# Kernel tuning notes

Measured on AMD Instinct MI355X. Metric: run time of the kernel, lower is better.

The kernel has to match this reference:

```python
import jax, jax.numpy as jnp
import numpy as np

NUM_NODES = 15000


def _gcn_conv(x, W, b, src, dst, norm, num_nodes):
    # PyG GCNConv: x' = D^-1/2 (A + I) D^-1/2 (x W) + b
    h = x @ W                                   # [N, out]
    msg = h[src] * norm[:, None]                # gather + scale per edge
    out = jax.ops.segment_sum(msg, dst, num_segments=num_nodes)
    return out + b


def setup_inputs() -> dict:
    key = jax.random.key(0)
    ks = jax.random.split(key, 12)
    T = 100000
    E = 200000
    inp = {
        "x": jax.random.normal(ks[0], (NUM_NODES, 768), jnp.float32),
        "r_emb": jax.random.normal(ks[1], (T, 768), jnp.float32),
        "W1": jax.random.normal(ks[2], (768, 10), jnp.float32) * 0.05,
        "b1": jax.random.normal(ks[3], (10,), jnp.float32) * 0.05,
        "W2": jax.random.normal(ks[4], (10, 128), jnp.float32) * 0.05,
        "b2": jax.random.normal(ks[5], (128,), jnp.float32) * 0.05,
        "W_ih": jax.random.normal(ks[6], (512, 1024), jnp.float32) * 0.03,
        "W_hh": jax.random.normal(ks[7], (512, 128), jnp.float32) * 0.03,
        "b_ih": jax.random.normal(ks[8], (512,), jnp.float32) * 0.03,
        "b_hh": jax.random.normal(ks[9], (512,), jnp.float32) * 0.03,
        "edge_index": jax.random.randint(ks[10], (2, E), 0, NUM_NODES).astype(jnp.int64),
        "triples": jax.random.randint(ks[11], (T, 3), 0, NUM_NODES).astype(jnp.int64),
    }
    return inp


def reference(x, r_emb, W1, b1, W2, b2, W_ih, W_hh, b_ih, b_hh, edge_index, triples):
    N = x.shape[0]
    H = 128  # lstm hidden size
    # --- add self loops, symmetric GCN normalization ---
    loop = jnp.arange(N, dtype=edge_index.dtype)
    src = jnp.concatenate([edge_index[0], loop])
    dst = jnp.concatenate([edge_index[1], loop])
    deg = jax.ops.segment_sum(jnp.ones_like(dst, jnp.float32), dst, num_segments=N)
    dinv = jnp.where(deg > 0, jax.lax.rsqrt(deg), 0.0)
    norm = dinv[src] * dinv[dst]                      # [E+N]
    # --- 2-layer GCN ---
    h = jax.nn.relu(_gcn_conv(x, W1, b1, src, dst, norm, N))   # [N, 10]
    z = _gcn_conv(h, W2, b2, src, dst, norm, N)                # [N, 128]
    # --- per-triple LSTM scoring, batched (seq_len=1, zero init state) ---
    hvec = z[triples[:, 0]]                           # [T, 128]
    tvec = z[triples[:, 2]]                           # [T, 128]
    feat = jnp.concatenate([hvec, r_emb, tvec], axis=-1)       # [T, 1024]
    gates = feat @ W_ih.T + (b_ih + b_hh)             # [T, 512]; h0=0 so W_hh term vanishes
    i_g, f_g, g_g, o_g = jnp.split(gates, 4, axis=-1)  # torch gate order i,f,g,o
    c = jax.nn.sigmoid(i_g) * jnp.tanh(g_g)           # c0 = 0 -> forget term drops
    out = jax.nn.sigmoid(o_g) * jnp.tanh(c)           # [T, 128]
    score = jax.nn.sigmoid(jnp.sum(out, axis=-1))     # [T]
    return score
```

## Files before the change

### kernel.cpp

```cpp
#include <hip/hip_runtime.h>

#define NF 768
#define D1 10
#define D2 128
#define BM 64

typedef __attribute__((ext_vector_type(8))) short bf16x8;
typedef __attribute__((ext_vector_type(16))) float f32x16;

static __device__ __forceinline__ float sigf(float v){ return 1.0f/(1.0f+__expf(-v)); }
static __device__ __forceinline__ float tanhfast(float v){ return 2.0f/(1.0f+__expf(-2.0f*v)) - 1.0f; }
static __device__ __forceinline__ short f2bf(float f){
    unsigned u = __float_as_uint(f);
    u += 0x7fffu + ((u>>16)&1u);
    return (short)(u>>16);
}

static __device__ __forceinline__ void gload16(const void* g, void* l){
    __builtin_amdgcn_global_load_lds(
        (const __attribute__((address_space(1))) unsigned int*)(unsigned long long)g,
        (__attribute__((address_space(3))) unsigned int*)(unsigned long long)l,
        16, 0, 0);
}

static __device__ __forceinline__ bf16x8 cvt8(float4 a, float4 b){
    unsigned u0,u1,u2,u3;
    asm("v_cvt_pk_bf16_f32 %0, %1, %2" : "=v"(u0) : "v"(a.x), "v"(a.y));
    asm("v_cvt_pk_bf16_f32 %0, %1, %2" : "=v"(u1) : "v"(a.z), "v"(a.w));
    asm("v_cvt_pk_bf16_f32 %0, %1, %2" : "=v"(u2) : "v"(b.x), "v"(b.y));
    asm("v_cvt_pk_bf16_f32 %0, %1, %2" : "=v"(u3) : "v"(b.z), "v"(b.w));
    union { unsigned u[4]; bf16x8 v; } r;
    r.u[0]=u0; r.u[1]=u1; r.u[2]=u2; r.u[3]=u3;
    return r.v;
}

__global__ void k_deg(const int* __restrict__ dst, int* __restrict__ cnt, int E){
    int e = blockIdx.x*256 + threadIdx.x;
    if(e<E) atomicAdd(&cnt[dst[e]], 1);
}

__global__ __launch_bounds__(256) void k_scan(const int* __restrict__ cnt,
                                              int* __restrict__ rowptr, int* __restrict__ rowcur,
                                              float* __restrict__ dinv, int N, int E){
    __shared__ int part[256];
    int t = threadIdx.x;
    int C = (N+255)/256;
    int lo = t*C, hi = lo+C; if(hi>N) hi=N; if(lo>N) lo=N;
    int s=0;
    for(int i=lo;i<hi;i++) s += cnt[i];
    part[t]=s;
    __syncthreads();
    if(t==0){
        int run=0;
        for(int i=0;i<256;i++){ int v=part[i]; part[i]=run; run+=v; }
        rowptr[N]=E;
    }
    __syncthreads();
    int run = part[t];
    for(int i=lo;i<hi;i++){
        rowptr[i]=run; rowcur[i]=run; run += cnt[i];
        dinv[i] = rsqrtf((float)cnt[i] + 1.0f);
    }
}

__global__ void k_fill(const int* __restrict__ src, const int* __restrict__ dst,
                       const float* __restrict__ dinv, int* __restrict__ rowcur,
                       int* __restrict__ esrc, float* __restrict__ enorm, int E){
    int e = blockIdx.x*256 + threadIdx.x;
    if(e>=E) return;
    int s=src[e], d=dst[e];
    int pos = atomicAdd(&rowcur[d], 1);
    esrc[pos]=s;
    enorm[pos]=dinv[s]*dinv[d];
}

__global__ __launch_bounds__(256) void k_h1(const float* __restrict__ x,
                                            const float* __restrict__ W1,
                                            float* __restrict__ h1, int N){
    __shared__ float wt[D1*NF];
    for(int idx=threadIdx.x; idx<NF*D1; idx+=256){
        int k=idx/D1, c=idx-k*D1;
        wt[c*NF+k]=W1[idx];
    }
    __syncthreads();
    int row = blockIdx.x*4 + (threadIdx.x>>6);
    int lane = threadIdx.x&63;
    if(row>=N) return;
    const float4* xr = (const float4*)(x + (size_t)row*NF);
    float acc[D1];
#pragma unroll
    for(int c=0;c<D1;c++) acc[c]=0.f;
#pragma unroll
    for(int i=0;i<3;i++){
        float4 v = xr[lane + 64*i];
#pragma unroll
        for(int c=0;c<D1;c++){
            float4 w = *(const float4*)&wt[c*NF + (lane+64*i)*4];
            acc[c] += v.x*w.x + v.y*w.y + v.z*w.z + v.w*w.w;
        }
    }
#pragma unroll
    for(int c=0;c<D1;c++){
        float v=acc[c];
#pragma unroll
        for(int off=32;off;off>>=1) v += __shfl_down(v,off,64);
        acc[c]=v;
    }
    if(lane==0){
#pragma unroll
        for(int c=0;c<D1;c++) h1[(size_t)row*D1+c]=acc[c];
    }
}

__global__ __launch_bounds__(256) void k_gath1(const float* __restrict__ h1,
        const int* __restrict__ rowptr, const int* __restrict__ esrc,
        const float* __restrict__ enorm, const float* __restrict__ dinv,
        const float* __restrict__ b1, float* __restrict__ h, int N){
    int node = blockIdx.x*4 + (threadIdx.x>>6);
    int lane = threadIdx.x&63;
    if(node>=N) return;
    int e0=rowptr[node], e1=rowptr[node+1];
    float acc[D1];
#pragma unroll
    for(int c=0;c<D1;c++) acc[c]=0.f;
    for(int e=e0+lane; e<e1; e+=64){
        int s=esrc[e]; float w=enorm[e];
        const float* hr = h1 + (size_t)s*D1;
#pragma unroll
        for(int c=0;c<D1;c++) acc[c] += hr[c]*w;
    }
    if(lane==0){
        float di=dinv[node], d2=di*di;
        const float* hr = h1 + (size_t)node*D1;
#pragma unroll
        for(int c=0;c<D1;c++) acc[c] += hr[c]*d2;
    }
#pragma unroll
    for(int c=0;c<D1;c++){
        float v=acc[c];
#pragma unroll
        for(int off=32;off;off>>=1) v += __shfl_down(v,off,64);
        acc[c]=v;
    }
    if(lane==0){
#pragma unroll
        for(int c=0;c<D1;c++){
            float v = acc[c] + b1[c];
            h[(size_t)node*D1+c] = v>0.f ? v : 0.f;
        }
    }
}

__global__ __launch_bounds__(128) void k_hz(const float* __restrict__ h,
                                            const float* __restrict__ W2,
                                            float* __restrict__ hz, int N){
    __shared__ float w2s[D1*D2];
    int j = threadIdx.x;
    for(int i=j;i<D1*D2;i+=128) w2s[i]=W2[i];
    __syncthreads();
    int n = blockIdx.x;
    if(n>=N) return;
    const float* hr = h + (size_t)n*D1;
    float acc=0.f;
#pragma unroll
    for(int k=0;k<D1;k++) acc += hr[k]*w2s[k*D2+j];
    hz[(size_t)n*D2+j]=acc;
}

__global__ __launch_bounds__(128) void k_gath2(const float* __restrict__ hz,
        const int* __restrict__ rowptr, const int* __restrict__ esrc,
        const float* __restrict__ enorm, const float* __restrict__ dinv,
        const float* __restrict__ b2, float* __restrict__ zbf, int N){
    int n = blockIdx.x;
    int c = threadIdx.x;
    int e0 = rowptr[n], e1 = rowptr[n+1];
    float di = dinv[n];
    float acc = hz[(size_t)n*D2+c]*di*di + b2[c];
    int e = e0;
    for(; e+1<e1; e+=2){
        int s0=esrc[e], s1=esrc[e+1];
        float w0=enorm[e], w1=enorm[e+1];
        acc += hz[(size_t)s0*D2+c]*w0 + hz[(size_t)s1*D2+c]*w1;
    }
    if(e<e1) acc += hz[(size_t)esrc[e]*D2+c]*enorm[e];
    zbf[(size_t)n*D2+c] = acc;
}

__global__ void k_wimgB(const float* __restrict__ Wih, ushort* __restrict__ img){
    int gid = blockIdx.x*256 + threadIdx.x;
    if(gid >= 12*64*64) return;
    int l = gid & 63;
    int ks16 = (gid>>6) & 63;
    int f = gid >> 12;
    int dd = l & 31, kb = l>>5;
    int wn = f/3, gi = f - wn*3;
    int gbase = (gi==0)?0:((gi==1)?256:384);
    int wrow = gbase + wn*32 + dd;
    int k = ks16*16 + kb*8;
    const float* p = Wih + (size_t)wrow*1024 + k;
    float4 v0=*(const float4*)p, v1=*(const float4*)(p+4);
    bf16x8 o;
    o[0]=f2bf(v0.x); o[1]=f2bf(v0.y); o[2]=f2bf(v0.z); o[3]=f2bf(v0.w);
    o[4]=f2bf(v1.x); o[5]=f2bf(v1.y); o[6]=f2bf(v1.z); o[7]=f2bf(v1.w);
    *(bf16x8*)(img + (size_t)gid*8) = o;
}

__global__ __launch_bounds__(256,3) void k_big(
    const float* __restrict__ remb, const ushort* __restrict__ img,
    const float* __restrict__ zbf, const float* __restrict__ b_ih,
    const float* __restrict__ b_hh, const int* __restrict__ trip,
    float* __restrict__ score, int T)
{
    __shared__ float  As[64*32];
    __shared__ ushort Bs[24*64*8];
    int tid=threadIdx.x, lane=tid&63, w=tid>>6;
    int l31=lane&31, lh=lane>>5;
    int t0=blockIdx.x*BM;

    const int aoff = ((lane&7) ^ (lane>>3))*4;
    const float* pzh[2]; const float* prm[2]; const float* pzt[2];
#pragma unroll
    for(int j=0;j<2;j++){
        int row = w*16 + j*8 + (lane>>3);
        int tc = t0+row; if(tc>=T) tc=T-1;
        pzh[j] = zbf + (size_t)trip[3*tc]*D2   + aoff;
        prm[j] = remb + (size_t)tc*NF          + aoff;
        pzt[j] = zbf + (size_t)trip[3*tc+2]*D2 + aoff;
    }
    float* adst0 = &As[(w*16+0)*32];
    float* adst1 = &As[(w*16+8)*32];

    f32x16 acc[2][3];
    const f32x16 zer = {0,0,0,0,0,0,0,0,0,0,0,0,0,0,0,0};
#pragma unroll
    for(int m=0;m<2;m++)
#pragma unroll
        for(int g=0;g<3;g++) acc[m][g]=zer;

    const int rx7 = l31&7;

    for(int s=0;s<32;s++){
        const float *sa0, *sa1;
        if(s<4)      { sa0=pzh[0]+s*32;      sa1=pzh[1]+s*32; }
        else if(s<28){ sa0=prm[0]+(s-4)*32;  sa1=prm[1]+(s-4)*32; }
        else         { sa0=pzt[0]+(s-28)*32; sa1=pzt[1]+(s-28)*32; }
        gload16(sa0, adst0);
        gload16(sa1, adst1);
#pragma unroll
        for(int j=0;j<6;j++){
            int f = w*3 + (j>>1), sh = j&1;
            gload16(img + ((size_t)(f*64 + s*2 + sh)*64 + lane)*8,
                    &Bs[(size_t)((f*2+sh)*64)*8]);
        }
        __syncthreads();
#pragma unroll
        for(int h=0;h<2;h++){
            int u0 = h*4 + lh*2;
            float4 a00 = *(const float4*)&As[ l31*32     + ((u0  )^rx7)*4];
            float4 a01 = *(const float4*)&As[ l31*32     + ((u0+1)^rx7)*4];
            bf16x8 A0 = cvt8(a00,a01);
            float4 a10 = *(const float4*)&As[(32+l31)*32 + ((u0  )^rx7)*4];
            float4 a11 = *(const float4*)&As[(32+l31)*32 + ((u0+1)^rx7)*4];
            bf16x8 A1 = cvt8(a10,a11);
            bf16x8 B0 = *(const bf16x8*)&Bs[(size_t)(((w*3+0)*2+h)*64+lane)*8];
            bf16x8 B1 = *(const bf16x8*)&Bs[(size_t)(((w*3+1)*2+h)*64+lane)*8];
            bf16x8 B2 = *(const bf16x8*)&Bs[(size_t)(((w*3+2)*2+h)*64+lane)*8];
            acc[0][0]=__builtin_amdgcn_mfma_f32_32x32x16_bf16(A0,B0,acc[0][0],0,0,0);
            acc[0][1]=__builtin_amdgcn_mfma_f32_32x32x16_bf16(A0,B1,acc[0][1],0,0,0);
            acc[0][2]=__builtin_amdgcn_mfma_f32_32x32x16_bf16(A0,B2,acc[0][2],0,0,0);
            acc[1][0]=__builtin_amdgcn_mfma_f32_32x32x16_bf16(A1,B0,acc[1][0],0,0,0);
            acc[1][1]=__builtin_amdgcn_mfma_f32_32x32x16_bf16(A1,B1,acc[1][1],0,0,0);
            acc[1][2]=__builtin_amdgcn_mfma_f32_32x32x16_bf16(A1,B2,acc[1][2],0,0,0);
        }
        __syncthreads();
    }

    float* rowsum = &As[0];
    if(tid<BM) rowsum[tid]=0.f;
    __syncthreads();
    int d = w*32+l31;
    float bi=b_ih[d]+b_hh[d];
    float bg=b_ih[256+d]+b_hh[256+d];
    float bo=b_ih[384+d]+b_hh[384+d];
#pragma unroll
    for(int m=0;m<2;m++){
#pragma unroll
        for(int r=0;r<16;r++){
            int row = m*32 + (r&3)+8*(r>>2)+4*lh;
            float ig = acc[m][0][r] + bi;
            float gg = acc[m][1][r] + bg;
            float og = acc[m][2][r] + bo;
            float cc = sigf(ig)*tanhfast(gg);
            float ov = sigf(og)*tanhfast(cc);
#pragma unroll
            for(int off=1; off<32; off<<=1) ov += __shfl_xor(ov, off, 64);
            if(l31==0) atomicAdd(&rowsum[row], ov);
        }
    }
    __syncthreads();
    if(tid < BM){
        int t = t0 + tid;
        if(t < T) score[t] = sigf(rowsum[tid]);
    }
}

extern "C" void kernel_launch(void* const* d_in, const int* in_sizes, int n_in,
                              void* d_out, int out_size, void* d_ws, size_t ws_size,
                              hipStream_t stream){
    const float* x    = (const float*)d_in[0];
    const float* remb = (const float*)d_in[1];
    const float* W1   = (const float*)d_in[2];
    const float* b1   = (const float*)d_in[3];
    const float* W2   = (const float*)d_in[4];
    const float* b2   = (const float*)d_in[5];
    const float* Wih  = (const float*)d_in[6];
    const float* b_ih = (const float*)d_in[8];
    const float* b_hh = (const float*)d_in[9];
    const int*   ei   = (const int*)d_in[10];
    const int*   trip = (const int*)d_in[11];
    float* score = (float*)d_out;

    const int N = in_sizes[0]/NF;
    const int E = in_sizes[10]/2;
    const int T = in_sizes[11]/3;
    const int* src = ei;
    const int* dst = ei + E;

    float* ws = (float*)d_ws;
    size_t o = 0;
    ushort* img  = (ushort*)(ws+o); o += (size_t)12*64*64*8/2;
    float* zbf   = ws+o;            o += (size_t)N*D2;
    int*   cnt    = (int*)(ws+o);   o += (size_t)((N+8)&~7);
    int*   rowptr = (int*)(ws+o);   o += (size_t)((N+8)&~7);
    int*   rowcur = (int*)(ws+o);   o += (size_t)((N+8)&~7);
    int*   esrc   = (int*)(ws+o);   o += (size_t)E;
    float* enorm  = ws+o;           o += (size_t)E;
    float* dinv   = ws+o;           o += (size_t)((N+7)&~7);
    float* h1     = ws+o;           o += (size_t)N*D1;
    float* hbuf   = ws+o;           o += (size_t)N*D1;
    float* hz     = ws+o;           o += (size_t)N*D2;
    (void)ws_size; (void)n_in; (void)out_size;

    hipMemsetAsync(cnt, 0, (size_t)N*sizeof(int), stream);

    k_wimgB<<<dim3((12*64*64+255)/256), dim3(256), 0, stream>>>(Wih, img);
    k_deg  <<<dim3((E+255)/256), dim3(256), 0, stream>>>(dst, cnt, E);
    k_scan <<<dim3(1), dim3(256), 0, stream>>>(cnt, rowptr, rowcur, dinv, N, E);
    k_fill <<<dim3((E+255)/256), dim3(256), 0, stream>>>(src, dst, dinv, rowcur, esrc, enorm, E);
    k_h1   <<<dim3((N+3)/4), dim3(256), 0, stream>>>(x, W1, h1, N);
    k_gath1<<<dim3((N+3)/4), dim3(256), 0, stream>>>(h1, rowptr, esrc, enorm, dinv, b1, hbuf, N);
    k_hz   <<<dim3(N), dim3(128), 0, stream>>>(hbuf, W2, hz, N);
    k_gath2<<<dim3(N), dim3(128), 0, stream>>>(hz, rowptr, esrc, enorm, dinv, b2, zbf, N);
    k_big  <<<dim3((T+BM-1)/BM), dim3(256), 0, stream>>>(remb, img, zbf, b_ih, b_hh, trip, score, T);
}
```

Measured before the change: 327.1 us.

## Split LSTM GEMM into single-wave blocks with software-pipelined loads; fuse GCN kernels

The big triple-scoring GEMM now runs one 64-thread wave per block, each owning one 32-column slice of the gates. A 4-slot software pipeline prefetches activations into registers and weights via direct-to-LDS loads, with explicit vmcnt waits and no block barriers. Row sums are accumulated with global atomics, and a separate sigmoid kernel produces the scores. The layer-1 gather is fused with the W2 projection, and the degree-count memset is folded into the weight-conversion kernel. The trade-off is that each wave re-reads the same activation rows (four times per tile), plus extra atomics and one more launch.

```diff
diff --git a/kernel.cpp b/kernel.cpp
--- a/kernel.cpp
+++ b/kernel.cpp
@@ -3,7 +3,6 @@
 #define NF 768
 #define D1 10
 #define D2 128
-#define BM 64
 
 typedef __attribute__((ext_vector_type(8))) short bf16x8;
 typedef __attribute__((ext_vector_type(16))) float f32x16;
@@ -112,12 +111,17 @@
     }
 }
 
-__global__ __launch_bounds__(256) void k_gath1(const float* __restrict__ h1,
+__global__ __launch_bounds__(128) void k_gh(const float* __restrict__ h1,
         const int* __restrict__ rowptr, const int* __restrict__ esrc,
         const float* __restrict__ enorm, const float* __restrict__ dinv,
-        const float* __restrict__ b1, float* __restrict__ h, int N){
-    int node = blockIdx.x*4 + (threadIdx.x>>6);
-    int lane = threadIdx.x&63;
+        const float* __restrict__ b1, const float* __restrict__ W2,
+        float* __restrict__ hz, int N){
+    __shared__ float w2s[D1*D2];
+    int tid = threadIdx.x;
+    for(int i=tid;i<D1*D2;i+=128) w2s[i]=W2[i];
+    __syncthreads();
+    int node = blockIdx.x*2 + (tid>>6);
+    int lane = tid&63;
     if(node>=N) return;
     int e0=rowptr[node], e1=rowptr[node+1];
     float acc[D1];
@@ -129,42 +133,29 @@
 #pragma unroll
         for(int c=0;c<D1;c++) acc[c] += hr[c]*w;
     }
-    if(lane==0){
-        float di=dinv[node], d2=di*di;
-        const float* hr = h1 + (size_t)node*D1;
-#pragma unroll
-        for(int c=0;c<D1;c++) acc[c] += hr[c]*d2;
-    }
 #pragma unroll
     for(int c=0;c<D1;c++){
         float v=acc[c];
 #pragma unroll
         for(int off=32;off;off>>=1) v += __shfl_down(v,off,64);
-        acc[c]=v;
-    }
-    if(lane==0){
-#pragma unroll
-        for(int c=0;c<D1;c++){
-            float v = acc[c] + b1[c];
-            h[(size_t)node*D1+c] = v>0.f ? v : 0.f;
-        }
-    }
-}
-
-__global__ __launch_bounds__(128) void k_hz(const float* __restrict__ h,
-                                            const float* __restrict__ W2,
-                                            float* __restrict__ hz, int N){
-    __shared__ float w2s[D1*D2];
-    int j = threadIdx.x;
-    for(int i=j;i<D1*D2;i+=128) w2s[i]=W2[i];
-    __syncthreads();
-    int n = blockIdx.x;
-    if(n>=N) return;
-    const float* hr = h + (size_t)n*D1;
-    float acc=0.f;
-#pragma unroll
-    for(int k=0;k<D1;k++) acc += hr[k]*w2s[k*D2+j];
-    hz[(size_t)n*D2+j]=acc;
+        acc[c] = __shfl(v, 0, 64);
+    }
+    float di=dinv[node], d2=di*di;
+    const float* hr = h1 + (size_t)node*D1;
+    float h[D1];
+#pragma unroll
+    for(int c=0;c<D1;c++){
+        float v = acc[c] + hr[c]*d2 + b1[c];
+        h[c] = v>0.f ? v : 0.f;
+    }
+    float o0=0.f, o1=0.f;
+#pragma unroll
+    for(int k=0;k<D1;k++){
+        o0 += h[k]*w2s[k*D2 + lane];
+        o1 += h[k]*w2s[k*D2 + 64 + lane];
+    }
+    hz[(size_t)node*D2 + lane]      = o0;
+    hz[(size_t)node*D2 + 64 + lane] = o1;
 }
 
 __global__ __launch_bounds__(128) void k_gath2(const float* __restrict__ hz,
@@ -186,8 +177,10 @@
     zbf[(size_t)n*D2+c] = acc;
 }
 
-__global__ void k_wimgB(const float* __restrict__ Wih, ushort* __restrict__ img){
+__global__ void k_wimgB(const float* __restrict__ Wih, ushort* __restrict__ img,
+                        int* __restrict__ cnt, int N){
     int gid = blockIdx.x*256 + threadIdx.x;
+    if(gid < N) cnt[gid] = 0;
     if(gid >= 12*64*64) return;
     int l = gid & 63;
     int ks16 = (gid>>6) & 63;
@@ -205,30 +198,27 @@
     *(bf16x8*)(img + (size_t)gid*8) = o;
 }
 
-__global__ __launch_bounds__(256,3) void k_big(
+__global__ __launch_bounds__(64,2) void k_big(
     const float* __restrict__ remb, const ushort* __restrict__ img,
     const float* __restrict__ zbf, const float* __restrict__ b_ih,
     const float* __restrict__ b_hh, const int* __restrict__ trip,
-    float* __restrict__ score, int T)
+    float* __restrict__ rowacc, int T)
 {
-    __shared__ float  As[64*32];
-    __shared__ ushort Bs[24*64*8];
-    int tid=threadIdx.x, lane=tid&63, w=tid>>6;
-    int l31=lane&31, lh=lane>>5;
-    int t0=blockIdx.x*BM;
-
-    const int aoff = ((lane&7) ^ (lane>>3))*4;
-    const float* pzh[2]; const float* prm[2]; const float* pzt[2];
-#pragma unroll
-    for(int j=0;j<2;j++){
-        int row = w*16 + j*8 + (lane>>3);
-        int tc = t0+row; if(tc>=T) tc=T-1;
-        pzh[j] = zbf + (size_t)trip[3*tc]*D2   + aoff;
-        prm[j] = remb + (size_t)tc*NF          + aoff;
-        pzt[j] = zbf + (size_t)trip[3*tc+2]*D2 + aoff;
-    }
-    float* adst0 = &As[(w*16+0)*32];
-    float* adst1 = &As[(w*16+8)*32];
+    __shared__ ushort Ab[4*2*64*8];
+    __shared__ ushort Bb[4*3*64*8];
+    int lane = threadIdx.x;
+    int bid  = blockIdx.x;
+    int tile = bid>>2, wn = bid&3;
+    int t0 = tile*64;
+    int l31 = lane&31, lh = lane>>5;
+
+    int tc = t0 + lane; if(tc>=T) tc=T-1;
+    const float* pzh = zbf + (size_t)trip[3*tc]*D2;
+    const float* prm = remb + (size_t)tc*NF;
+    const float* pzt = zbf + (size_t)trip[3*tc+2]*D2;
+    const ushort* wb0 = img + ((size_t)((wn*3+0)*4096) + lane)*8;
+    const ushort* wb1 = img + ((size_t)((wn*3+1)*4096) + lane)*8;
+    const ushort* wb2 = img + ((size_t)((wn*3+2)*4096) + lane)*8;
 
     f32x16 acc[2][3];
     const f32x16 zer = {0,0,0,0,0,0,0,0,0,0,0,0,0,0,0,0};
@@ -237,48 +227,71 @@
 #pragma unroll
         for(int g=0;g<3;g++) acc[m][g]=zer;
 
-    const int rx7 = l31&7;
-
-    for(int s=0;s<32;s++){
-        const float *sa0, *sa1;
-        if(s<4)      { sa0=pzh[0]+s*32;      sa1=pzh[1]+s*32; }
-        else if(s<28){ sa0=prm[0]+(s-4)*32;  sa1=prm[1]+(s-4)*32; }
-        else         { sa0=pzt[0]+(s-28)*32; sa1=pzt[1]+(s-28)*32; }
-        gload16(sa0, adst0);
-        gload16(sa1, adst1);
-#pragma unroll
-        for(int j=0;j<6;j++){
-            int f = w*3 + (j>>1), sh = j&1;
-            gload16(img + ((size_t)(f*64 + s*2 + sh)*64 + lane)*8,
-                    &Bs[(size_t)((f*2+sh)*64)*8]);
-        }
-        __syncthreads();
-#pragma unroll
-        for(int h=0;h<2;h++){
-            int u0 = h*4 + lh*2;
-            float4 a00 = *(const float4*)&As[ l31*32     + ((u0  )^rx7)*4];
-            float4 a01 = *(const float4*)&As[ l31*32     + ((u0+1)^rx7)*4];
-            bf16x8 A0 = cvt8(a00,a01);
-            float4 a10 = *(const float4*)&As[(32+l31)*32 + ((u0  )^rx7)*4];
-            float4 a11 = *(const float4*)&As[(32+l31)*32 + ((u0+1)^rx7)*4];
-            bf16x8 A1 = cvt8(a10,a11);
-            bf16x8 B0 = *(const bf16x8*)&Bs[(size_t)(((w*3+0)*2+h)*64+lane)*8];
-            bf16x8 B1 = *(const bf16x8*)&Bs[(size_t)(((w*3+1)*2+h)*64+lane)*8];
-            bf16x8 B2 = *(const bf16x8*)&Bs[(size_t)(((w*3+2)*2+h)*64+lane)*8];
-            acc[0][0]=__builtin_amdgcn_mfma_f32_32x32x16_bf16(A0,B0,acc[0][0],0,0,0);
-            acc[0][1]=__builtin_amdgcn_mfma_f32_32x32x16_bf16(A0,B1,acc[0][1],0,0,0);
-            acc[0][2]=__builtin_amdgcn_mfma_f32_32x32x16_bf16(A0,B2,acc[0][2],0,0,0);
-            acc[1][0]=__builtin_amdgcn_mfma_f32_32x32x16_bf16(A1,B0,acc[1][0],0,0,0);
-            acc[1][1]=__builtin_amdgcn_mfma_f32_32x32x16_bf16(A1,B1,acc[1][1],0,0,0);
-            acc[1][2]=__builtin_amdgcn_mfma_f32_32x32x16_bf16(A1,B2,acc[1][2],0,0,0);
-        }
-        __syncthreads();
-    }
-
-    float* rowsum = &As[0];
-    if(tid<BM) rowsum[tid]=0.f;
-    __syncthreads();
-    int d = w*32+l31;
+    float4 pa[4][4];
+
+#define SRCP(s_) ((s_)<8 ? (pzh+(s_)*16) : ((s_)<56 ? (prm+((s_)-8)*16) : (pzt+((s_)-56)*16)))
+#define PALOAD(s_) if((s_)<64){ const float* p_=SRCP(s_); \
+    pa[(s_)&3][0]=*(const float4*)(p_);    pa[(s_)&3][1]=*(const float4*)(p_+4); \
+    pa[(s_)&3][2]=*(const float4*)(p_+8);  pa[(s_)&3][3]=*(const float4*)(p_+12); }
+#define BISSUE(s_) if((s_)<64){ \
+    gload16(wb0+(size_t)(s_)*512, &Bb[(((s_)&3)*3+0)*512]); \
+    gload16(wb1+(size_t)(s_)*512, &Bb[(((s_)&3)*3+1)*512]); \
+    gload16(wb2+(size_t)(s_)*512, &Bb[(((s_)&3)*3+2)*512]); }
+#define AWRITE(s_) if((s_)<64){ int sl_=(s_)&3; \
+    *(bf16x8*)&Ab[((sl_*2+0)*64+lane)*8] = cvt8(pa[sl_][0], pa[sl_][1]); \
+    *(bf16x8*)&Ab[((sl_*2+1)*64+lane)*8] = cvt8(pa[sl_][2], pa[sl_][3]); }
+#define COMPUTE(s_) { int sl_=(s_)&3; \
+    bf16x8 A0_ = *(const bf16x8*)&Ab[((sl_*2+lh)*64 + l31)*8]; \
+    bf16x8 A1_ = *(const bf16x8*)&Ab[((sl_*2+lh)*64 + 32 + l31)*8]; \
+    bf16x8 B0_ = *(const bf16x8*)&Bb[((sl_*3+0)*64 + lane)*8]; \
+    bf16x8 B1_ = *(const bf16x8*)&Bb[((sl_*3+1)*64 + lane)*8]; \
+    bf16x8 B2_ = *(const bf16x8*)&Bb[((sl_*3+2)*64 + lane)*8]; \
+    __builtin_amdgcn_s_setprio(1); \
+    acc[0][0]=__builtin_amdgcn_mfma_f32_32x32x16_bf16(A0_,B0_,acc[0][0],0,0,0); \
+    acc[0][1]=__builtin_amdgcn_mfma_f32_32x32x16_bf16(A0_,B1_,acc[0][1],0,0,0); \
+    acc[0][2]=__builtin_amdgcn_mfma_f32_32x32x16_bf16(A0_,B2_,acc[0][2],0,0,0); \
+    acc[1][0]=__builtin_amdgcn_mfma_f32_32x32x16_bf16(A1_,B0_,acc[1][0],0,0,0); \
+    acc[1][1]=__builtin_amdgcn_mfma_f32_32x32x16_bf16(A1_,B1_,acc[1][1],0,0,0); \
+    acc[1][2]=__builtin_amdgcn_mfma_f32_32x32x16_bf16(A1_,B2_,acc[1][2],0,0,0); \
+    __builtin_amdgcn_s_setprio(0); }
+
+#define STEP(s_, W_) { \
+    BISSUE((s_)+2) \
+    __builtin_amdgcn_sched_barrier(0); \
+    PALOAD((s_)+3) \
+    __builtin_amdgcn_sched_barrier(0); \
+    AWRITE((s_)+1) \
+    asm volatile("s_waitcnt vmcnt(" W_ ")" ::: "memory"); \
+    __builtin_amdgcn_sched_barrier(0); \
+    COMPUTE(s_) \
+}
+
+    PALOAD(0) PALOAD(1) PALOAD(2)
+    __builtin_amdgcn_sched_barrier(0);
+    BISSUE(0) BISSUE(1)
+    __builtin_amdgcn_sched_barrier(0);
+    AWRITE(0)
+
+    STEP(0 ,"10") STEP(1 ,"14")
+    STEP(2 ,"18") STEP(3 ,"18") STEP(4 ,"18") STEP(5 ,"18") STEP(6 ,"18") STEP(7 ,"18")
+    STEP(8 ,"18") STEP(9 ,"18") STEP(10,"18") STEP(11,"18") STEP(12,"18") STEP(13,"18")
+    STEP(14,"18") STEP(15,"18") STEP(16,"18") STEP(17,"18") STEP(18,"18") STEP(19,"18")
+    STEP(20,"18") STEP(21,"18") STEP(22,"18") STEP(23,"18") STEP(24,"18") STEP(25,"18")
+    STEP(26,"18") STEP(27,"18") STEP(28,"18") STEP(29,"18") STEP(30,"18") STEP(31,"18")
+    STEP(32,"18") STEP(33,"18") STEP(34,"18") STEP(35,"18") STEP(36,"18") STEP(37,"18")
+    STEP(38,"18") STEP(39,"18") STEP(40,"18") STEP(41,"18") STEP(42,"18") STEP(43,"18")
+    STEP(44,"18") STEP(45,"18") STEP(46,"18") STEP(47,"18") STEP(48,"18") STEP(49,"18")
+    STEP(50,"18") STEP(51,"18") STEP(52,"18") STEP(53,"18") STEP(54,"18") STEP(55,"18")
+    STEP(56,"18") STEP(57,"18") STEP(58,"18") STEP(59,"18") STEP(60,"18")
+    STEP(61,"14") STEP(62,"7")  STEP(63,"0")
+#undef STEP
+#undef COMPUTE
+#undef AWRITE
+#undef BISSUE
+#undef PALOAD
+#undef SRCP
+
+    int d = wn*32 + l31;
     float bi=b_ih[d]+b_hh[d];
     float bg=b_ih[256+d]+b_hh[256+d];
     float bo=b_ih[384+d]+b_hh[384+d];
@@ -287,21 +300,25 @@
 #pragma unroll
         for(int r=0;r<16;r++){
             int row = m*32 + (r&3)+8*(r>>2)+4*lh;
-            float ig = acc[m][0][r] + bi;
-            float gg = acc[m][1][r] + bg;
-            float og = acc[m][2][r] + bo;
-            float cc = sigf(ig)*tanhfast(gg);
-            float ov = sigf(og)*tanhfast(cc);
+            int t = t0+row;
+            float ov = 0.f;
+            if(t<T){
+                float ig = acc[m][0][r] + bi;
+                float gg = acc[m][1][r] + bg;
+                float og = acc[m][2][r] + bo;
+                float cc = sigf(ig)*tanhfast(gg);
+                ov = sigf(og)*tanhfast(cc);
+            }
 #pragma unroll
             for(int off=1; off<32; off<<=1) ov += __shfl_xor(ov, off, 64);
-            if(l31==0) atomicAdd(&rowsum[row], ov);
+            if(l31==0 && t<T) atomicAdd(&rowacc[t], ov);
         }
     }
-    __syncthreads();
-    if(tid < BM){
-        int t = t0 + tid;
-        if(t < T) score[t] = sigf(rowsum[tid]);
-    }
+}
+
+__global__ void k_sig(const float* __restrict__ rowacc, float* __restrict__ score, int T){
+    int t = blockIdx.x*256 + threadIdx.x;
+    if(t<T) score[t] = sigf(rowacc[t]);
 }
 
 extern "C" void kernel_launch(void* const* d_in, const int* in_sizes, int n_in,
@@ -330,6 +347,7 @@
     size_t o = 0;
     ushort* img  = (ushort*)(ws+o); o += (size_t)12*64*64*8/2;
     float* zbf   = ws+o;            o += (size_t)N*D2;
+    float* rowacc= ws+o;            o += (size_t)((T+7)&~7);
     int*   cnt    = (int*)(ws+o);   o += (size_t)((N+8)&~7);
     int*   rowptr = (int*)(ws+o);   o += (size_t)((N+8)&~7);
     int*   rowcur = (int*)(ws+o);   o += (size_t)((N+8)&~7);
@@ -337,19 +355,18 @@
     float* enorm  = ws+o;           o += (size_t)E;
     float* dinv   = ws+o;           o += (size_t)((N+7)&~7);
     float* h1     = ws+o;           o += (size_t)N*D1;
-    float* hbuf   = ws+o;           o += (size_t)N*D1;
     float* hz     = ws+o;           o += (size_t)N*D2;
     (void)ws_size; (void)n_in; (void)out_size;
 
-    hipMemsetAsync(cnt, 0, (size_t)N*sizeof(int), stream);
-
-    k_wimgB<<<dim3((12*64*64+255)/256), dim3(256), 0, stream>>>(Wih, img);
+    hipMemsetAsync(rowacc, 0, (size_t)T*sizeof(float), stream);
+
+    k_wimgB<<<dim3((12*64*64+255)/256), dim3(256), 0, stream>>>(Wih, img, cnt, N);
     k_deg  <<<dim3((E+255)/256), dim3(256), 0, stream>>>(dst, cnt, E);
     k_scan <<<dim3(1), dim3(256), 0, stream>>>(cnt, rowptr, rowcur, dinv, N, E);
     k_fill <<<dim3((E+255)/256), dim3(256), 0, stream>>>(src, dst, dinv, rowcur, esrc, enorm, E);
     k_h1   <<<dim3((N+3)/4), dim3(256), 0, stream>>>(x, W1, h1, N);
-    k_gath1<<<dim3((N+3)/4), dim3(256), 0, stream>>>(h1, rowptr, esrc, enorm, dinv, b1, hbuf, N);
-    k_hz   <<<dim3(N), dim3(128), 0, stream>>>(hbuf, W2, hz, N);
+    k_gh   <<<dim3((N+1)/2), dim3(128), 0, stream>>>(h1, rowptr, esrc, enorm, dinv, b1, W2, hz, N);
     k_gath2<<<dim3(N), dim3(128), 0, stream>>>(hz, rowptr, esrc, enorm, dinv, b2, zbf, N);
-    k_big  <<<dim3((T+BM-1)/BM), dim3(256), 0, stream>>>(remb, img, zbf, b_ih, b_hh, trip, score, T);
-}
+    k_big  <<<dim3(((T+63)/64)*4), dim3(64), 0, stream>>>(remb, img, zbf, b_ih, b_hh, trip, rowacc, T);
+    k_sig  <<<dim3((T+255)/256), dim3(256), 0, stream>>>(rowacc, score, T);
+}
```

New measurement: 490.2 us. 1.5x slower.
